# Kernel optimization log

Measured on AMD Instinct MI355X. Metric: run time of the kernel, lower is better.

The kernel has to match this reference:

```python
import jax, jax.numpy as jnp
import numpy as np

N_NODES = 50000
HIDDEN = 64
N_EDGES = 800000
HOPS = (1, 2, 3)


def setup_inputs() -> dict:
    key = jax.random.key(0)
    ks = jax.random.split(key, 16)
    d = HIDDEN
    inp = {
        "x": jax.random.normal(ks[0], (N_NODES, d), dtype=jnp.float32),
        "edge_index": jax.random.randint(ks[1], (2, N_EDGES), 0, N_NODES, dtype=jnp.int64),
    }
    s = 1.0 / np.sqrt(d)
    # per-hop GIN MLP params: Linear(d,d) -> ReLU -> Linear(d,d)
    for i in range(len(HOPS)):
        inp[f"W1_{i}"] = jax.random.uniform(ks[2 + 4 * i], (d, d), jnp.float32, -s, s)
        inp[f"b1_{i}"] = jax.random.uniform(ks[3 + 4 * i], (d,), jnp.float32, -s, s)
        inp[f"W2_{i}"] = jax.random.uniform(ks[4 + 4 * i], (d, d), jnp.float32, -s, s)
        inp[f"b2_{i}"] = jax.random.uniform(ks[5 + 4 * i], (d,), jnp.float32, -s, s)
    so = 1.0 / np.sqrt(d * len(HOPS))
    inp["Wo"] = jax.random.uniform(ks[14], (d * len(HOPS), d), jnp.float32, -so, so)
    inp["bo"] = jax.random.uniform(ks[15], (d,), jnp.float32, -so, so)
    return inp


def _gin_conv(h, src, dst, W1, b1, W2, b2):
    # GINConv with eps=0: MLP(x + sum_{j in N(i)} x_j)
    agg = jax.ops.segment_sum(h[src], dst, num_segments=N_NODES)  # [N, d]
    z = h + agg
    z = jax.nn.relu(z @ W1 + b1) @ W2 + b2
    return z


def reference(x, edge_index,
              W1_0, b1_0, W2_0, b2_0,
              W1_1, b1_1, W2_1, b2_1,
              W1_2, b1_2, W2_2, b2_2,
              Wo, bo):
    src, dst = edge_index[0], edge_index[1]
    params = [(W1_0, b1_0, W2_0, b2_0),
              (W1_1, b1_1, W2_1, b2_1),
              (W1_2, b1_2, W2_2, b2_2)]
    outs = []
    for hop, (W1, b1, W2, b2) in zip(HOPS, params):
        h = x
        for _ in range(hop):
            h = _gin_conv(h, src, dst, W1, b1, W2, b2)
        outs.append(h)
    return jnp.concatenate(outs, axis=-1) @ Wo + bo
```

## Files before the change

### kernel.cpp

```cpp
#include <hip/hip_runtime.h>

#define NN 50000
#define NE 800000
#define D  64
#define TILE 64
#define TPB 512
#define KTOT 192
#define NBLK 196


__global__ __launch_bounds__(256) void k_zero(int* __restrict__ p, int n) {
    int i = blockIdx.x * 256 + threadIdx.x;
    if (i < n) p[i] = 0;
}

__global__ __launch_bounds__(256) void k_count(const int* __restrict__ ei, int* __restrict__ deg) {
    int e = blockIdx.x * 256 + threadIdx.x;
    if (e < NE) atomicAdd(&deg[ei[NE + e]], 1);
}

__global__ __launch_bounds__(256) void k_bsum(const int* __restrict__ deg, int* __restrict__ bsum) {
    __shared__ int s[256];
    int t = threadIdx.x;
    int i = blockIdx.x * 256 + t;
    s[t] = (i < NN) ? deg[i] : 0;
    __syncthreads();
    for (int off = 128; off > 0; off >>= 1) {
        if (t < off) s[t] += s[t + off];
        __syncthreads();
    }
    if (t == 0) bsum[blockIdx.x] = s[0];
}

__global__ __launch_bounds__(256) void k_boff(const int* __restrict__ bsum,
                                              int* __restrict__ boff,
                                              int* __restrict__ row_ptr) {
    __shared__ int s[256];
    int t = threadIdx.x;
    int v = (t < NBLK) ? bsum[t] : 0;
    s[t] = v;
    __syncthreads();
    for (int off = 1; off < 256; off <<= 1) {
        int u = (t >= off) ? s[t - off] : 0;
        __syncthreads();
        s[t] += u;
        __syncthreads();
    }
    boff[t] = s[t] - v;
    if (t == 0) row_ptr[NN] = NE;
}

__global__ __launch_bounds__(256) void k_scan2(const int* __restrict__ deg,
                                               const int* __restrict__ boff,
                                               int* __restrict__ row_ptr,
                                               int* __restrict__ cursor) {
    __shared__ int s[256];
    int t = threadIdx.x;
    int i = blockIdx.x * 256 + t;
    int v = (i < NN) ? deg[i] : 0;
    s[t] = v;
    __syncthreads();
    for (int off = 1; off < 256; off <<= 1) {
        int u = (t >= off) ? s[t - off] : 0;
        __syncthreads();
        s[t] += u;
        __syncthreads();
    }
    int excl = s[t] - v + boff[blockIdx.x];
    if (i < NN) { row_ptr[i] = excl; cursor[i] = excl; }
}

__global__ __launch_bounds__(256) void k_fill(const int* __restrict__ ei,
                                              int* __restrict__ cursor,
                                              int* __restrict__ colv) {
    int e = blockIdx.x * 256 + threadIdx.x;
    if (e < NE) {
        int d = ei[NE + e];
        int p = atomicAdd(&cursor[d], 1);
        colv[p] = ei[e];
    }
}


__device__ __forceinline__ float4 gather_row(const float4* __restrict__ h4,
                                             const int* __restrict__ row_ptr,
                                             const int* __restrict__ colv,
                                             int n, int g, int q) {
    float4 a0 = make_float4(0.f, 0.f, 0.f, 0.f);
    float4 a1 = make_float4(0.f, 0.f, 0.f, 0.f);
    float4 a2 = make_float4(0.f, 0.f, 0.f, 0.f);
    float4 a3 = make_float4(0.f, 0.f, 0.f, 0.f);
    if (n >= 0) {
        if (g == 0) a0 = h4[n * 16 + q];
        int e1 = row_ptr[n + 1];
        int e  = row_ptr[n] + g;
        for (; e + 12 < e1; e += 16) {
            int s0 = colv[e], s1 = colv[e + 4], s2 = colv[e + 8], s3 = colv[e + 12];
            float4 v0 = h4[s0 * 16 + q];
            float4 v1 = h4[s1 * 16 + q];
            float4 v2 = h4[s2 * 16 + q];
            float4 v3 = h4[s3 * 16 + q];
            a0.x += v0.x; a0.y += v0.y; a0.z += v0.z; a0.w += v0.w;
            a1.x += v1.x; a1.y += v1.y; a1.z += v1.z; a1.w += v1.w;
            a2.x += v2.x; a2.y += v2.y; a2.z += v2.z; a2.w += v2.w;
            a3.x += v3.x; a3.y += v3.y; a3.z += v3.z; a3.w += v3.w;
        }
        for (; e < e1; e += 4) {
            float4 v = h4[colv[e] * 16 + q];
            a1.x += v.x; a1.y += v.y; a1.z += v.z; a1.w += v.w;
        }
        a0.x += a1.x + a2.x + a3.x;
        a0.y += a1.y + a2.y + a3.y;
        a0.z += a1.z + a2.z + a3.z;
        a0.w += a1.w + a2.w + a3.w;
    }
    a0.x += __shfl_xor(a0.x, 16); a0.y += __shfl_xor(a0.y, 16);
    a0.z += __shfl_xor(a0.z, 16); a0.w += __shfl_xor(a0.w, 16);
    a0.x += __shfl_xor(a0.x, 32); a0.y += __shfl_xor(a0.y, 32);
    a0.z += __shfl_xor(a0.z, 32); a0.w += __shfl_xor(a0.w, 32);
    return a0;
}


__global__ __launch_bounds__(TPB) void k_conv(
    const float4* __restrict__ h4,
    const int* __restrict__ row_ptr,
    const int* __restrict__ colv,
    const float* __restrict__ W1, const float* __restrict__ b1,
    const float* __restrict__ W2, const float* __restrict__ b2,
    float4* __restrict__ out4)
{
    __shared__ float sW1[D][D];
    __shared__ float sW2[D][D];
    __shared__ float4 sZ4[TILE][17];
    __shared__ float sB1[D], sB2[D];

    int tid = threadIdx.x;
    int node0 = blockIdx.x * TILE;

    {
        const float4* w14 = (const float4*)W1;
        const float4* w24 = (const float4*)W2;
        float4* s14 = (float4*)sW1;
        float4* s24 = (float4*)sW2;
        for (int i = tid; i < D * D / 4; i += TPB) { s14[i] = w14[i]; s24[i] = w24[i]; }
        if (tid < D) { sB1[tid] = b1[tid]; sB2[tid] = b2[tid]; }
    }

    int wave = tid >> 6, lane = tid & 63;
    int g = lane >> 4, q = lane & 15;

    for (int r = wave; r < TILE; r += (TPB / 64)) {
        int n = node0 + r;
        float4 a = gather_row(h4, row_ptr, colv, (n < NN) ? n : -1, g, q);
        if (g == 0) sZ4[r][q] = a;
    }
    __syncthreads();

    int tr = tid >> 4, tc = tid & 15;
    float* zr0 = (float*)&sZ4[tr * 2 + 0][0];
    float* zr1 = (float*)&sZ4[tr * 2 + 1][0];

    float acc[2][4];
    #pragma unroll
    for (int c = 0; c < 4; ++c) { acc[0][c] = sB1[tc * 4 + c]; acc[1][c] = sB1[tc * 4 + c]; }
    #pragma unroll 16
    for (int k = 0; k < D; ++k) {
        float z0 = zr0[k], z1 = zr1[k];
        #pragma unroll
        for (int c = 0; c < 4; ++c) {
            float w = sW1[k][tc * 4 + c];
            acc[0][c] += z0 * w;
            acc[1][c] += z1 * w;
        }
    }
    {
        float4 h0, h1;
        h0.x = fmaxf(acc[0][0], 0.f); h0.y = fmaxf(acc[0][1], 0.f);
        h0.z = fmaxf(acc[0][2], 0.f); h0.w = fmaxf(acc[0][3], 0.f);
        h1.x = fmaxf(acc[1][0], 0.f); h1.y = fmaxf(acc[1][1], 0.f);
        h1.z = fmaxf(acc[1][2], 0.f); h1.w = fmaxf(acc[1][3], 0.f);
        *(float4*)&zr0[tc * 4] = h0;
        *(float4*)&zr1[tc * 4] = h1;
    }
    #pragma unroll
    for (int c = 0; c < 4; ++c) { acc[0][c] = sB2[tc * 4 + c]; acc[1][c] = sB2[tc * 4 + c]; }
    #pragma unroll 16
    for (int k = 0; k < D; ++k) {
        float z0 = zr0[k], z1 = zr1[k];
        #pragma unroll
        for (int c = 0; c < 4; ++c) {
            float w = sW2[k][tc * 4 + c];
            acc[0][c] += z0 * w;
            acc[1][c] += z1 * w;
        }
    }
    #pragma unroll
    for (int i = 0; i < 2; ++i) {
        int n = node0 + tr * 2 + i;
        if (n < NN) {
            float4 o;
            o.x = acc[i][0]; o.y = acc[i][1]; o.z = acc[i][2]; o.w = acc[i][3];
            out4[n * 16 + tc] = o;
        }
    }
}


__global__ __launch_bounds__(TPB) void k_aggmlp3(
    const float4* __restrict__ h4,
    const int* __restrict__ row_ptr,
    const int* __restrict__ colv,
    const float* __restrict__ W1a, const float* __restrict__ b1a,
    const float* __restrict__ W2a, const float* __restrict__ b2a,
    const float* __restrict__ W1b, const float* __restrict__ b1b,
    const float* __restrict__ W2b, const float* __restrict__ b2b,
    const float* __restrict__ W1c, const float* __restrict__ b1c,
    const float* __restrict__ W2c, const float* __restrict__ b2c,
    float4* __restrict__ outA, float4* __restrict__ outB, float4* __restrict__ outC)
{
    __shared__ float sW[D][D];
    __shared__ float4 sZ4[TILE][17];
    __shared__ float4 sH4[TILE][17];
    __shared__ float sB[D];

    int tid = threadIdx.x;
    int node0 = blockIdx.x * TILE;

    int wave = tid >> 6, lane = tid & 63;
    int g = lane >> 4, q = lane & 63 & 15;

    for (int r = wave; r < TILE; r += (TPB / 64)) {
        int n = node0 + r;
        float4 a = gather_row(h4, row_ptr, colv, (n < NN) ? n : -1, g, q);
        if (g == 0) sZ4[r][q] = a;
    }

    int tr = tid >> 4, tc = tid & 15;
    float* zr0 = (float*)&sZ4[tr * 2 + 0][0];
    float* zr1 = (float*)&sZ4[tr * 2 + 1][0];
    float* hr0 = (float*)&sH4[tr * 2 + 0][0];
    float* hr1 = (float*)&sH4[tr * 2 + 1][0];

    #pragma unroll 1
    for (int m = 0; m < 3; ++m) {
        const float* W1 = (m == 0) ? W1a : (m == 1) ? W1b : W1c;
        const float* B1 = (m == 0) ? b1a : (m == 1) ? b1b : b1c;
        const float* W2 = (m == 0) ? W2a : (m == 1) ? W2b : W2c;
        const float* B2 = (m == 0) ? b2a : (m == 1) ? b2b : b2c;
        float4* out4 = (m == 0) ? outA : (m == 1) ? outB : outC;

        {
            const float4* w4 = (const float4*)W1;
            float4* s4 = (float4*)sW;
            for (int i = tid; i < D * D / 4; i += TPB) s4[i] = w4[i];
            if (tid < D) sB[tid] = B1[tid];
        }
        __syncthreads();

        float acc[2][4];
        #pragma unroll
        for (int c = 0; c < 4; ++c) { acc[0][c] = sB[tc * 4 + c]; acc[1][c] = sB[tc * 4 + c]; }
        #pragma unroll 16
        for (int k = 0; k < D; ++k) {
            float z0 = zr0[k], z1 = zr1[k];
            #pragma unroll
            for (int c = 0; c < 4; ++c) {
                float w = sW[k][tc * 4 + c];
                acc[0][c] += z0 * w;
                acc[1][c] += z1 * w;
            }
        }
        {
            float4 h0, h1;
            h0.x = fmaxf(acc[0][0], 0.f); h0.y = fmaxf(acc[0][1], 0.f);
            h0.z = fmaxf(acc[0][2], 0.f); h0.w = fmaxf(acc[0][3], 0.f);
            h1.x = fmaxf(acc[1][0], 0.f); h1.y = fmaxf(acc[1][1], 0.f);
            h1.z = fmaxf(acc[1][2], 0.f); h1.w = fmaxf(acc[1][3], 0.f);
            *(float4*)&hr0[tc * 4] = h0;
            *(float4*)&hr1[tc * 4] = h1;
        }
        __syncthreads();

        {
            const float4* w4 = (const float4*)W2;
            float4* s4 = (float4*)sW;
            for (int i = tid; i < D * D / 4; i += TPB) s4[i] = w4[i];
            if (tid < D) sB[tid] = B2[tid];
        }
        __syncthreads();

        #pragma unroll
        for (int c = 0; c < 4; ++c) { acc[0][c] = sB[tc * 4 + c]; acc[1][c] = sB[tc * 4 + c]; }
        #pragma unroll 16
        for (int k = 0; k < D; ++k) {
            float h0 = hr0[k], h1 = hr1[k];
            #pragma unroll
            for (int c = 0; c < 4; ++c) {
                float w = sW[k][tc * 4 + c];
                acc[0][c] += h0 * w;
                acc[1][c] += h1 * w;
            }
        }
        #pragma unroll
        for (int i = 0; i < 2; ++i) {
            int n = node0 + tr * 2 + i;
            if (n < NN) {
                float4 o;
                o.x = acc[i][0]; o.y = acc[i][1]; o.z = acc[i][2]; o.w = acc[i][3];
                out4[n * 16 + tc] = o;
            }
        }
        __syncthreads();
    }
}


__global__ __launch_bounds__(TPB) void k_final(
    const float4* __restrict__ H0, const float4* __restrict__ H1,
    const float4* __restrict__ H2,
    const float* __restrict__ Wo, const float* __restrict__ bo,
    float4* __restrict__ out4)
{
    __shared__ float4 sW4[KTOT * 16];
    __shared__ float4 sZ4[TILE][49];
    __shared__ float sB[D];

    int tid = threadIdx.x;
    int node0 = blockIdx.x * TILE;

    {
        const float4* w4 = (const float4*)Wo;
        for (int i = tid; i < KTOT * 16; i += TPB) sW4[i] = w4[i];
        if (tid < D) sB[tid] = bo[tid];
    }

    int wave = tid >> 6, lane = tid & 63;
    int part = lane >> 4, q = lane & 15;
    for (int r = wave; r < TILE; r += (TPB / 64)) {
        int n = node0 + r;
        if (part < 3) {
            float4 v = make_float4(0.f, 0.f, 0.f, 0.f);
            if (n < NN) {
                const float4* hp = (part == 0) ? H0 : (part == 1) ? H1 : H2;
                v = hp[n * 16 + q];
            }
            sZ4[r][part * 16 + q] = v;
        }
    }
    __syncthreads();

    const float* sW = (const float*)sW4;
    int tr = tid >> 4, tc = tid & 15;
    const float* zr0 = (const float*)&sZ4[tr * 2 + 0][0];
    const float* zr1 = (const float*)&sZ4[tr * 2 + 1][0];

    float acc[2][4];
    #pragma unroll
    for (int c = 0; c < 4; ++c) { acc[0][c] = sB[tc * 4 + c]; acc[1][c] = sB[tc * 4 + c]; }
    #pragma unroll 8
    for (int k = 0; k < KTOT; ++k) {
        float z0 = zr0[k], z1 = zr1[k];
        #pragma unroll
        for (int c = 0; c < 4; ++c) {
            float w = sW[k * 64 + tc * 4 + c];
            acc[0][c] += z0 * w;
            acc[1][c] += z1 * w;
        }
    }
    #pragma unroll
    for (int i = 0; i < 2; ++i) {
        int n = node0 + tr * 2 + i;
        if (n < NN) {
            float4 o;
            o.x = acc[i][0]; o.y = acc[i][1]; o.z = acc[i][2]; o.w = acc[i][3];
            out4[n * 16 + tc] = o;
        }
    }
}


extern "C" void kernel_launch(void* const* d_in, const int* in_sizes, int n_in,
                              void* d_out, int out_size, void* d_ws, size_t ws_size,
                              hipStream_t stream) {
    const float* x    = (const float*)d_in[0];
    const int*   ei   = (const int*)d_in[1];
    const float* W1_0 = (const float*)d_in[2];
    const float* b1_0 = (const float*)d_in[3];
    const float* W2_0 = (const float*)d_in[4];
    const float* b2_0 = (const float*)d_in[5];
    const float* W1_1 = (const float*)d_in[6];
    const float* b1_1 = (const float*)d_in[7];
    const float* W2_1 = (const float*)d_in[8];
    const float* b2_1 = (const float*)d_in[9];
    const float* W1_2 = (const float*)d_in[10];
    const float* b1_2 = (const float*)d_in[11];
    const float* W2_2 = (const float*)d_in[12];
    const float* b2_2 = (const float*)d_in[13];
    const float* Wo   = (const float*)d_in[14];
    const float* bo   = (const float*)d_in[15];
    float4* out = (float4*)d_out;

    char* ws = (char*)d_ws;
    int* deg     = (int*)(ws + 0);
    int* cursor  = (int*)(ws + 200704);
    int* row_ptr = (int*)(ws + 401408);
    int* colv    = (int*)(ws + 602112);
    int* bsum    = (int*)(ws + 3802112);
    int* boff    = (int*)(ws + 3803136);
    float* fbase = (float*)(ws + 3804160);
    float4* H0 = (float4*)(fbase);
    float4* H1 = (float4*)(fbase + 3200000);
    float4* H2 = (float4*)(fbase + 6400000);
    float4* tA = (float4*)(fbase + 9600000);
    const float4* x4 = (const float4*)x;

    k_zero <<<NBLK, 256, 0, stream>>>(deg, NN);
    k_count<<<(NE + 255) / 256, 256, 0, stream>>>(ei, deg);
    k_bsum <<<NBLK, 256, 0, stream>>>(deg, bsum);
    k_boff <<<1, 256, 0, stream>>>(bsum, boff, row_ptr);
    k_scan2<<<NBLK, 256, 0, stream>>>(deg, boff, row_ptr, cursor);
    k_fill <<<(NE + 255) / 256, 256, 0, stream>>>(ei, cursor, colv);

    int nb = (NN + TILE - 1) / TILE;

    k_aggmlp3<<<nb, TPB, 0, stream>>>(x4, row_ptr, colv,
                                      W1_0, b1_0, W2_0, b2_0,
                                      W1_1, b1_1, W2_1, b2_1,
                                      W1_2, b1_2, W2_2, b2_2,
                                      H0, tA, out);

    k_conv<<<nb, TPB, 0, stream>>>((const float4*)tA, row_ptr, colv,
                                   W1_1, b1_1, W2_1, b2_1, H1);

    k_conv<<<nb, TPB, 0, stream>>>((const float4*)out, row_ptr, colv,
                                   W1_2, b1_2, W2_2, b2_2, tA);
    k_conv<<<nb, TPB, 0, stream>>>((const float4*)tA, row_ptr, colv,
                                   W1_2, b1_2, W2_2, b2_2, H2);

    k_final<<<nb, TPB, 0, stream>>>((const float4*)H0, (const float4*)H1, (const float4*)H2,
                                    Wo, bo, out);
}
```

Measured before the change: 397.5 us.

## Fuse hop-2 convs into dual-gather kernel and fold output projection into last conv

Merges the two independent second-round GIN convolutions (hop-2 second layer and hop-3 second layer) into one kernel that gathers both feature tensors in the same edge loop, sharing the colv index reads. The final hop-3 conv is fused with the output projection, so H2 is never written to global memory and the projection streams Wo in three 64-row slices through one shared buffer. The device zeroing kernel is replaced by hipMemsetAsync. This cuts the launch count and the global traffic for edge indices and intermediates, at the cost of more serialized weight loads and syncs per block and a shallower gather unroll.

```diff
diff --git a/kernel.cpp b/kernel.cpp
--- a/kernel.cpp
+++ b/kernel.cpp
@@ -5,14 +5,8 @@
 #define D  64
 #define TILE 64
 #define TPB 512
-#define KTOT 192
 #define NBLK 196
 
-
-__global__ __launch_bounds__(256) void k_zero(int* __restrict__ p, int n) {
-    int i = blockIdx.x * 256 + threadIdx.x;
-    if (i < n) p[i] = 0;
-}
 
 __global__ __launch_bounds__(256) void k_count(const int* __restrict__ ei, int* __restrict__ deg) {
     int e = blockIdx.x * 256 + threadIdx.x;
@@ -81,6 +75,54 @@
     }
 }
 
+
+__device__ __forceinline__ void load_w(float (&sW)[D][D], const float* __restrict__ W, int tid) {
+    const float4* w4 = (const float4*)W;
+    float4* s4 = (float4*)sW;
+    for (int i = tid; i < D * D / 4; i += TPB) s4[i] = w4[i];
+}
+
+__device__ __forceinline__ void acc_init(float acc[2][4], const float* sB, int tc) {
+    #pragma unroll
+    for (int c = 0; c < 4; ++c) { acc[0][c] = sB[tc * 4 + c]; acc[1][c] = sB[tc * 4 + c]; }
+}
+
+__device__ __forceinline__ void layer_acc(float acc[2][4], const float* zr0, const float* zr1,
+                                          const float (&sW)[D][D], int tc) {
+    #pragma unroll 16
+    for (int k = 0; k < D; ++k) {
+        float z0 = zr0[k], z1 = zr1[k];
+        #pragma unroll
+        for (int c = 0; c < 4; ++c) {
+            float w = sW[k][tc * 4 + c];
+            acc[0][c] += z0 * w;
+            acc[1][c] += z1 * w;
+        }
+    }
+}
+
+__device__ __forceinline__ void relu_wb(float acc[2][4], float* zr0, float* zr1, int tc) {
+    float4 h0, h1;
+    h0.x = fmaxf(acc[0][0], 0.f); h0.y = fmaxf(acc[0][1], 0.f);
+    h0.z = fmaxf(acc[0][2], 0.f); h0.w = fmaxf(acc[0][3], 0.f);
+    h1.x = fmaxf(acc[1][0], 0.f); h1.y = fmaxf(acc[1][1], 0.f);
+    h1.z = fmaxf(acc[1][2], 0.f); h1.w = fmaxf(acc[1][3], 0.f);
+    *(float4*)&zr0[tc * 4] = h0;
+    *(float4*)&zr1[tc * 4] = h1;
+}
+
+__device__ __forceinline__ void store_rows(float acc[2][4], float4* __restrict__ out4,
+                                           int node0, int tr, int tc) {
+    #pragma unroll
+    for (int i = 0; i < 2; ++i) {
+        int n = node0 + tr * 2 + i;
+        if (n < NN) {
+            float4 o;
+            o.x = acc[i][0]; o.y = acc[i][1]; o.z = acc[i][2]; o.w = acc[i][3];
+            out4[n * 16 + tc] = o;
+        }
+    }
+}
 
 __device__ __forceinline__ float4 gather_row(const float4* __restrict__ h4,
                                              const int* __restrict__ row_ptr,
@@ -122,91 +164,6 @@
 }
 
 
-__global__ __launch_bounds__(TPB) void k_conv(
-    const float4* __restrict__ h4,
-    const int* __restrict__ row_ptr,
-    const int* __restrict__ colv,
-    const float* __restrict__ W1, const float* __restrict__ b1,
-    const float* __restrict__ W2, const float* __restrict__ b2,
-    float4* __restrict__ out4)
-{
-    __shared__ float sW1[D][D];
-    __shared__ float sW2[D][D];
-    __shared__ float4 sZ4[TILE][17];
-    __shared__ float sB1[D], sB2[D];
-
-    int tid = threadIdx.x;
-    int node0 = blockIdx.x * TILE;
-
-    {
-        const float4* w14 = (const float4*)W1;
-        const float4* w24 = (const float4*)W2;
-        float4* s14 = (float4*)sW1;
-        float4* s24 = (float4*)sW2;
-        for (int i = tid; i < D * D / 4; i += TPB) { s14[i] = w14[i]; s24[i] = w24[i]; }
-        if (tid < D) { sB1[tid] = b1[tid]; sB2[tid] = b2[tid]; }
-    }
-
-    int wave = tid >> 6, lane = tid & 63;
-    int g = lane >> 4, q = lane & 15;
-
-    for (int r = wave; r < TILE; r += (TPB / 64)) {
-        int n = node0 + r;
-        float4 a = gather_row(h4, row_ptr, colv, (n < NN) ? n : -1, g, q);
-        if (g == 0) sZ4[r][q] = a;
-    }
-    __syncthreads();
-
-    int tr = tid >> 4, tc = tid & 15;
-    float* zr0 = (float*)&sZ4[tr * 2 + 0][0];
-    float* zr1 = (float*)&sZ4[tr * 2 + 1][0];
-
-    float acc[2][4];
-    #pragma unroll
-    for (int c = 0; c < 4; ++c) { acc[0][c] = sB1[tc * 4 + c]; acc[1][c] = sB1[tc * 4 + c]; }
-    #pragma unroll 16
-    for (int k = 0; k < D; ++k) {
-        float z0 = zr0[k], z1 = zr1[k];
-        #pragma unroll
-        for (int c = 0; c < 4; ++c) {
-            float w = sW1[k][tc * 4 + c];
-            acc[0][c] += z0 * w;
-            acc[1][c] += z1 * w;
-        }
-    }
-    {
-        float4 h0, h1;
-        h0.x = fmaxf(acc[0][0], 0.f); h0.y = fmaxf(acc[0][1], 0.f);
-        h0.z = fmaxf(acc[0][2], 0.f); h0.w = fmaxf(acc[0][3], 0.f);
-        h1.x = fmaxf(acc[1][0], 0.f); h1.y = fmaxf(acc[1][1], 0.f);
-        h1.z = fmaxf(acc[1][2], 0.f); h1.w = fmaxf(acc[1][3], 0.f);
-        *(float4*)&zr0[tc * 4] = h0;
-        *(float4*)&zr1[tc * 4] = h1;
-    }
-    #pragma unroll
-    for (int c = 0; c < 4; ++c) { acc[0][c] = sB2[tc * 4 + c]; acc[1][c] = sB2[tc * 4 + c]; }
-    #pragma unroll 16
-    for (int k = 0; k < D; ++k) {
-        float z0 = zr0[k], z1 = zr1[k];
-        #pragma unroll
-        for (int c = 0; c < 4; ++c) {
-            float w = sW2[k][tc * 4 + c];
-            acc[0][c] += z0 * w;
-            acc[1][c] += z1 * w;
-        }
-    }
-    #pragma unroll
-    for (int i = 0; i < 2; ++i) {
-        int n = node0 + tr * 2 + i;
-        if (n < NN) {
-            float4 o;
-            o.x = acc[i][0]; o.y = acc[i][1]; o.z = acc[i][2]; o.w = acc[i][3];
-            out4[n * 16 + tc] = o;
-        }
-    }
-}
-
-
 __global__ __launch_bounds__(TPB) void k_aggmlp3(
     const float4* __restrict__ h4,
     const int* __restrict__ row_ptr,
@@ -226,9 +183,8 @@
 
     int tid = threadIdx.x;
     int node0 = blockIdx.x * TILE;
-
     int wave = tid >> 6, lane = tid & 63;
-    int g = lane >> 4, q = lane & 63 & 15;
+    int g = lane >> 4, q = lane & 15;
 
     for (int r = wave; r < TILE; r += (TPB / 64)) {
         int n = node0 + r;
@@ -250,133 +206,201 @@
         const float* B2 = (m == 0) ? b2a : (m == 1) ? b2b : b2c;
         float4* out4 = (m == 0) ? outA : (m == 1) ? outB : outC;
 
-        {
-            const float4* w4 = (const float4*)W1;
-            float4* s4 = (float4*)sW;
-            for (int i = tid; i < D * D / 4; i += TPB) s4[i] = w4[i];
-            if (tid < D) sB[tid] = B1[tid];
+        load_w(sW, W1, tid);
+        if (tid < D) sB[tid] = B1[tid];
+        __syncthreads();
+
+        float acc[2][4];
+        acc_init(acc, sB, tc);
+        layer_acc(acc, zr0, zr1, sW, tc);
+        relu_wb(acc, hr0, hr1, tc);
+        __syncthreads();
+
+        load_w(sW, W2, tid);
+        if (tid < D) sB[tid] = B2[tid];
+        __syncthreads();
+
+        acc_init(acc, sB, tc);
+        layer_acc(acc, hr0, hr1, sW, tc);
+        store_rows(acc, out4, node0, tr, tc);
+        __syncthreads();
+    }
+}
+
+
+__global__ __launch_bounds__(TPB) void k_conv2(
+    const float4* __restrict__ hA4, const float4* __restrict__ hB4,
+    const int* __restrict__ row_ptr, const int* __restrict__ colv,
+    const float* __restrict__ W1a, const float* __restrict__ b1a,
+    const float* __restrict__ W2a, const float* __restrict__ b2a,
+    const float* __restrict__ W1b, const float* __restrict__ b1b,
+    const float* __restrict__ W2b, const float* __restrict__ b2b,
+    float4* __restrict__ outA4, float4* __restrict__ outB4)
+{
+    __shared__ float sW[D][D];
+    __shared__ float4 sZa[TILE][17];
+    __shared__ float4 sZb[TILE][17];
+    __shared__ float sB[D];
+
+    int tid = threadIdx.x;
+    int node0 = blockIdx.x * TILE;
+    int wave = tid >> 6, lane = tid & 63;
+    int g = lane >> 4, q = lane & 15;
+
+    for (int r = wave; r < TILE; r += (TPB / 64)) {
+        int n = node0 + r;
+        float4 a0 = make_float4(0.f, 0.f, 0.f, 0.f);
+        float4 a1 = make_float4(0.f, 0.f, 0.f, 0.f);
+        float4 b0 = make_float4(0.f, 0.f, 0.f, 0.f);
+        float4 b1v = make_float4(0.f, 0.f, 0.f, 0.f);
+        if (n < NN) {
+            if (g == 0) { a0 = hA4[n * 16 + q]; b0 = hB4[n * 16 + q]; }
+            int e1 = row_ptr[n + 1];
+            int e  = row_ptr[n] + g;
+            for (; e + 4 < e1; e += 8) {
+                int s0 = colv[e], s1 = colv[e + 4];
+                float4 va0 = hA4[s0 * 16 + q];
+                float4 vb0 = hB4[s0 * 16 + q];
+                float4 va1 = hA4[s1 * 16 + q];
+                float4 vb1 = hB4[s1 * 16 + q];
+                a0.x += va0.x; a0.y += va0.y; a0.z += va0.z; a0.w += va0.w;
+                b0.x += vb0.x; b0.y += vb0.y; b0.z += vb0.z; b0.w += vb0.w;
+                a1.x += va1.x; a1.y += va1.y; a1.z += va1.z; a1.w += va1.w;
+                b1v.x += vb1.x; b1v.y += vb1.y; b1v.z += vb1.z; b1v.w += vb1.w;
+            }
+            if (e < e1) {
+                int s = colv[e];
+                float4 va = hA4[s * 16 + q];
+                float4 vb = hB4[s * 16 + q];
+                a0.x += va.x; a0.y += va.y; a0.z += va.z; a0.w += va.w;
+                b0.x += vb.x; b0.y += vb.y; b0.z += vb.z; b0.w += vb.w;
+            }
+            a0.x += a1.x; a0.y += a1.y; a0.z += a1.z; a0.w += a1.w;
+            b0.x += b1v.x; b0.y += b1v.y; b0.z += b1v.z; b0.w += b1v.w;
         }
-        __syncthreads();
-
-        float acc[2][4];
-        #pragma unroll
-        for (int c = 0; c < 4; ++c) { acc[0][c] = sB[tc * 4 + c]; acc[1][c] = sB[tc * 4 + c]; }
-        #pragma unroll 16
-        for (int k = 0; k < D; ++k) {
-            float z0 = zr0[k], z1 = zr1[k];
-            #pragma unroll
-            for (int c = 0; c < 4; ++c) {
-                float w = sW[k][tc * 4 + c];
-                acc[0][c] += z0 * w;
-                acc[1][c] += z1 * w;
-            }
-        }
-        {
-            float4 h0, h1;
-            h0.x = fmaxf(acc[0][0], 0.f); h0.y = fmaxf(acc[0][1], 0.f);
-            h0.z = fmaxf(acc[0][2], 0.f); h0.w = fmaxf(acc[0][3], 0.f);
-            h1.x = fmaxf(acc[1][0], 0.f); h1.y = fmaxf(acc[1][1], 0.f);
-            h1.z = fmaxf(acc[1][2], 0.f); h1.w = fmaxf(acc[1][3], 0.f);
-            *(float4*)&hr0[tc * 4] = h0;
-            *(float4*)&hr1[tc * 4] = h1;
-        }
-        __syncthreads();
-
-        {
-            const float4* w4 = (const float4*)W2;
-            float4* s4 = (float4*)sW;
-            for (int i = tid; i < D * D / 4; i += TPB) s4[i] = w4[i];
-            if (tid < D) sB[tid] = B2[tid];
-        }
-        __syncthreads();
-
-        #pragma unroll
-        for (int c = 0; c < 4; ++c) { acc[0][c] = sB[tc * 4 + c]; acc[1][c] = sB[tc * 4 + c]; }
-        #pragma unroll 16
-        for (int k = 0; k < D; ++k) {
-            float h0 = hr0[k], h1 = hr1[k];
-            #pragma unroll
-            for (int c = 0; c < 4; ++c) {
-                float w = sW[k][tc * 4 + c];
-                acc[0][c] += h0 * w;
-                acc[1][c] += h1 * w;
-            }
-        }
-        #pragma unroll
-        for (int i = 0; i < 2; ++i) {
-            int n = node0 + tr * 2 + i;
-            if (n < NN) {
-                float4 o;
-                o.x = acc[i][0]; o.y = acc[i][1]; o.z = acc[i][2]; o.w = acc[i][3];
-                out4[n * 16 + tc] = o;
-            }
-        }
-        __syncthreads();
-    }
-}
-
-
-__global__ __launch_bounds__(TPB) void k_final(
+        a0.x += __shfl_xor(a0.x, 16); a0.y += __shfl_xor(a0.y, 16);
+        a0.z += __shfl_xor(a0.z, 16); a0.w += __shfl_xor(a0.w, 16);
+        a0.x += __shfl_xor(a0.x, 32); a0.y += __shfl_xor(a0.y, 32);
+        a0.z += __shfl_xor(a0.z, 32); a0.w += __shfl_xor(a0.w, 32);
+        b0.x += __shfl_xor(b0.x, 16); b0.y += __shfl_xor(b0.y, 16);
+        b0.z += __shfl_xor(b0.z, 16); b0.w += __shfl_xor(b0.w, 16);
+        b0.x += __shfl_xor(b0.x, 32); b0.y += __shfl_xor(b0.y, 32);
+        b0.z += __shfl_xor(b0.z, 32); b0.w += __shfl_xor(b0.w, 32);
+        if (g == 0) { sZa[r][q] = a0; sZb[r][q] = b0; }
+    }
+
+    int tr = tid >> 4, tc = tid & 15;
+    float* zra0 = (float*)&sZa[tr * 2 + 0][0];
+    float* zra1 = (float*)&sZa[tr * 2 + 1][0];
+    float* zrb0 = (float*)&sZb[tr * 2 + 0][0];
+    float* zrb1 = (float*)&sZb[tr * 2 + 1][0];
+    float acc[2][4];
+
+    load_w(sW, W1a, tid); if (tid < D) sB[tid] = b1a[tid];
+    __syncthreads();
+    acc_init(acc, sB, tc);
+    layer_acc(acc, zra0, zra1, sW, tc);
+    relu_wb(acc, zra0, zra1, tc);
+    __syncthreads();
+    load_w(sW, W2a, tid); if (tid < D) sB[tid] = b2a[tid];
+    __syncthreads();
+    acc_init(acc, sB, tc);
+    layer_acc(acc, zra0, zra1, sW, tc);
+    store_rows(acc, outA4, node0, tr, tc);
+    __syncthreads();
+
+    load_w(sW, W1b, tid); if (tid < D) sB[tid] = b1b[tid];
+    __syncthreads();
+    acc_init(acc, sB, tc);
+    layer_acc(acc, zrb0, zrb1, sW, tc);
+    relu_wb(acc, zrb0, zrb1, tc);
+    __syncthreads();
+    load_w(sW, W2b, tid); if (tid < D) sB[tid] = b2b[tid];
+    __syncthreads();
+    acc_init(acc, sB, tc);
+    layer_acc(acc, zrb0, zrb1, sW, tc);
+    store_rows(acc, outB4, node0, tr, tc);
+}
+
+
+__global__ __launch_bounds__(TPB) void k_conv_final(
+    const float4* __restrict__ h4,
     const float4* __restrict__ H0, const float4* __restrict__ H1,
-    const float4* __restrict__ H2,
+    const int* __restrict__ row_ptr, const int* __restrict__ colv,
+    const float* __restrict__ W1, const float* __restrict__ b1,
+    const float* __restrict__ W2, const float* __restrict__ b2,
     const float* __restrict__ Wo, const float* __restrict__ bo,
     float4* __restrict__ out4)
 {
-    __shared__ float4 sW4[KTOT * 16];
-    __shared__ float4 sZ4[TILE][49];
+    __shared__ float sW[D][D];
+    __shared__ float4 sZ4[TILE][17];
+    __shared__ float4 sY4[TILE][17];
     __shared__ float sB[D];
 
     int tid = threadIdx.x;
     int node0 = blockIdx.x * TILE;
-
-    {
-        const float4* w4 = (const float4*)Wo;
-        for (int i = tid; i < KTOT * 16; i += TPB) sW4[i] = w4[i];
-        if (tid < D) sB[tid] = bo[tid];
-    }
-
     int wave = tid >> 6, lane = tid & 63;
-    int part = lane >> 4, q = lane & 15;
+    int g = lane >> 4, q = lane & 15;
+
     for (int r = wave; r < TILE; r += (TPB / 64)) {
         int n = node0 + r;
-        if (part < 3) {
-            float4 v = make_float4(0.f, 0.f, 0.f, 0.f);
-            if (n < NN) {
-                const float4* hp = (part == 0) ? H0 : (part == 1) ? H1 : H2;
-                v = hp[n * 16 + q];
-            }
-            sZ4[r][part * 16 + q] = v;
-        }
-    }
-    __syncthreads();
-
-    const float* sW = (const float*)sW4;
+        float4 a = gather_row(h4, row_ptr, colv, (n < NN) ? n : -1, g, q);
+        if (g == 0) sZ4[r][q] = a;
+    }
+
     int tr = tid >> 4, tc = tid & 15;
-    const float* zr0 = (const float*)&sZ4[tr * 2 + 0][0];
-    const float* zr1 = (const float*)&sZ4[tr * 2 + 1][0];
-
+    float* zr0 = (float*)&sZ4[tr * 2 + 0][0];
+    float* zr1 = (float*)&sZ4[tr * 2 + 1][0];
+    float* yr0 = (float*)&sY4[tr * 2 + 0][0];
+    float* yr1 = (float*)&sY4[tr * 2 + 1][0];
     float acc[2][4];
-    #pragma unroll
-    for (int c = 0; c < 4; ++c) { acc[0][c] = sB[tc * 4 + c]; acc[1][c] = sB[tc * 4 + c]; }
-    #pragma unroll 8
-    for (int k = 0; k < KTOT; ++k) {
-        float z0 = zr0[k], z1 = zr1[k];
-        #pragma unroll
-        for (int c = 0; c < 4; ++c) {
-            float w = sW[k * 64 + tc * 4 + c];
-            acc[0][c] += z0 * w;
-            acc[1][c] += z1 * w;
-        }
-    }
-    #pragma unroll
-    for (int i = 0; i < 2; ++i) {
-        int n = node0 + tr * 2 + i;
-        if (n < NN) {
-            float4 o;
-            o.x = acc[i][0]; o.y = acc[i][1]; o.z = acc[i][2]; o.w = acc[i][3];
-            out4[n * 16 + tc] = o;
-        }
-    }
+
+    load_w(sW, W1, tid); if (tid < D) sB[tid] = b1[tid];
+    __syncthreads();
+    acc_init(acc, sB, tc);
+    layer_acc(acc, zr0, zr1, sW, tc);
+    relu_wb(acc, zr0, zr1, tc);
+    __syncthreads();
+    load_w(sW, W2, tid); if (tid < D) sB[tid] = b2[tid];
+    __syncthreads();
+    acc_init(acc, sB, tc);
+    layer_acc(acc, zr0, zr1, sW, tc);
+    {
+        float4 h0v, h1v;
+        h0v.x = acc[0][0]; h0v.y = acc[0][1]; h0v.z = acc[0][2]; h0v.w = acc[0][3];
+        h1v.x = acc[1][0]; h1v.y = acc[1][1]; h1v.z = acc[1][2]; h1v.w = acc[1][3];
+        *(float4*)&zr0[tc * 4] = h0v;
+        *(float4*)&zr1[tc * 4] = h1v;
+    }
+    __syncthreads();
+
+    load_w(sW, Wo + 128 * D, tid); if (tid < D) sB[tid] = bo[tid];
+    for (int i = tid; i < TILE * 16; i += TPB) {
+        int r = i >> 4, qq = i & 15;
+        int n = node0 + r;
+        sY4[r][qq] = (n < NN) ? H0[n * 16 + qq] : make_float4(0.f, 0.f, 0.f, 0.f);
+    }
+    __syncthreads();
+    float accO[2][4];
+    acc_init(accO, sB, tc);
+    layer_acc(accO, zr0, zr1, sW, tc);
+    __syncthreads();
+
+    load_w(sW, Wo, tid);
+    __syncthreads();
+    layer_acc(accO, yr0, yr1, sW, tc);
+    __syncthreads();
+
+    load_w(sW, Wo + 64 * D, tid);
+    for (int i = tid; i < TILE * 16; i += TPB) {
+        int r = i >> 4, qq = i & 15;
+        int n = node0 + r;
+        sY4[r][qq] = (n < NN) ? H1[n * 16 + qq] : make_float4(0.f, 0.f, 0.f, 0.f);
+    }
+    __syncthreads();
+    layer_acc(accO, yr0, yr1, sW, tc);
+
+    store_rows(accO, out4, node0, tr, tc);
 }
 
 
@@ -409,13 +433,13 @@
     int* bsum    = (int*)(ws + 3802112);
     int* boff    = (int*)(ws + 3803136);
     float* fbase = (float*)(ws + 3804160);
-    float4* H0 = (float4*)(fbase);
-    float4* H1 = (float4*)(fbase + 3200000);
-    float4* H2 = (float4*)(fbase + 6400000);
-    float4* tA = (float4*)(fbase + 9600000);
+    float4* H0  = (float4*)(fbase);
+    float4* H1  = (float4*)(fbase + 3200000);
+    float4* tB  = (float4*)(fbase + 6400000);
+    float4* tC2 = (float4*)(fbase + 9600000);
     const float4* x4 = (const float4*)x;
 
-    k_zero <<<NBLK, 256, 0, stream>>>(deg, NN);
+    hipMemsetAsync(deg, 0, NN * sizeof(int), stream);
     k_count<<<(NE + 255) / 256, 256, 0, stream>>>(ei, deg);
     k_bsum <<<NBLK, 256, 0, stream>>>(deg, bsum);
     k_boff <<<1, 256, 0, stream>>>(bsum, boff, row_ptr);
@@ -428,16 +452,16 @@
                                       W1_0, b1_0, W2_0, b2_0,
                                       W1_1, b1_1, W2_1, b2_1,
                                       W1_2, b1_2, W2_2, b2_2,
-                                      H0, tA, out);
-
-    k_conv<<<nb, TPB, 0, stream>>>((const float4*)tA, row_ptr, colv,
-                                   W1_1, b1_1, W2_1, b2_1, H1);
-
-    k_conv<<<nb, TPB, 0, stream>>>((const float4*)out, row_ptr, colv,
-                                   W1_2, b1_2, W2_2, b2_2, tA);
-    k_conv<<<nb, TPB, 0, stream>>>((const float4*)tA, row_ptr, colv,
-                                   W1_2, b1_2, W2_2, b2_2, H2);
-
-    k_final<<<nb, TPB, 0, stream>>>((const float4*)H0, (const float4*)H1, (const float4*)H2,
-                                    Wo, bo, out);
-}
+                                      H0, tB, out);
+
+    k_conv2<<<nb, TPB, 0, stream>>>(tB, (const float4*)out, row_ptr, colv,
+                                    W1_1, b1_1, W2_1, b2_1,
+                                    W1_2, b1_2, W2_2, b2_2,
+                                    H1, tC2);
+
+    k_conv_final<<<nb, TPB, 0, stream>>>((const float4*)tC2,
+                                         (const float4*)H0, (const float4*)H1,
+                                         row_ptr, colv,
+                                         W1_2, b1_2, W2_2, b2_2,
+                                         Wo, bo, out);
+}
```

After: 502.8 us. +26.5%, slower.

## Fuse last GIN conv with final output projection and replace zero kernel with memset

Applied to the files above, without the earlier changes.

Merges the third hop's final GINConv with the concatenated output projection into one kernel. The hop-3 result is kept in shared memory and multiplied by its slice of Wo, and H0 and H1 are reloaded per tile for the other two slices. This removes one kernel launch and the write and re-read of the H2 intermediate. The zeroing kernel is also replaced with hipMemsetAsync. In exchange, the fused kernel reloads a weight matrix into shared memory four times per tile and adds more barriers.

```diff
diff --git a/kernel.cpp b/kernel.cpp
--- a/kernel.cpp
+++ b/kernel.cpp
@@ -5,14 +5,8 @@
 #define D  64
 #define TILE 64
 #define TPB 512
-#define KTOT 192
 #define NBLK 196
 
-
-__global__ __launch_bounds__(256) void k_zero(int* __restrict__ p, int n) {
-    int i = blockIdx.x * 256 + threadIdx.x;
-    if (i < n) p[i] = 0;
-}
 
 __global__ __launch_bounds__(256) void k_count(const int* __restrict__ ei, int* __restrict__ deg) {
     int e = blockIdx.x * 256 + threadIdx.x;
@@ -316,64 +310,172 @@
 }
 
 
-__global__ __launch_bounds__(TPB) void k_final(
+__global__ __launch_bounds__(TPB) void k_conv_final(
+    const float4* __restrict__ h4,
     const float4* __restrict__ H0, const float4* __restrict__ H1,
-    const float4* __restrict__ H2,
+    const int* __restrict__ row_ptr, const int* __restrict__ colv,
+    const float* __restrict__ W1, const float* __restrict__ b1,
+    const float* __restrict__ W2, const float* __restrict__ b2,
     const float* __restrict__ Wo, const float* __restrict__ bo,
     float4* __restrict__ out4)
 {
-    __shared__ float4 sW4[KTOT * 16];
-    __shared__ float4 sZ4[TILE][49];
+    __shared__ float sW[D][D];
+    __shared__ float4 sZ4[TILE][17];
+    __shared__ float4 sY4[TILE][17];
     __shared__ float sB[D];
 
     int tid = threadIdx.x;
     int node0 = blockIdx.x * TILE;
-
-    {
-        const float4* w4 = (const float4*)Wo;
-        for (int i = tid; i < KTOT * 16; i += TPB) sW4[i] = w4[i];
-        if (tid < D) sB[tid] = bo[tid];
-    }
-
     int wave = tid >> 6, lane = tid & 63;
-    int part = lane >> 4, q = lane & 15;
+    int g = lane >> 4, q = lane & 15;
+
     for (int r = wave; r < TILE; r += (TPB / 64)) {
         int n = node0 + r;
-        if (part < 3) {
-            float4 v = make_float4(0.f, 0.f, 0.f, 0.f);
-            if (n < NN) {
-                const float4* hp = (part == 0) ? H0 : (part == 1) ? H1 : H2;
-                v = hp[n * 16 + q];
-            }
-            sZ4[r][part * 16 + q] = v;
-        }
-    }
-    __syncthreads();
-
-    const float* sW = (const float*)sW4;
+        float4 a = gather_row(h4, row_ptr, colv, (n < NN) ? n : -1, g, q);
+        if (g == 0) sZ4[r][q] = a;
+    }
+
     int tr = tid >> 4, tc = tid & 15;
-    const float* zr0 = (const float*)&sZ4[tr * 2 + 0][0];
-    const float* zr1 = (const float*)&sZ4[tr * 2 + 1][0];
+    float* zr0 = (float*)&sZ4[tr * 2 + 0][0];
+    float* zr1 = (float*)&sZ4[tr * 2 + 1][0];
+    float* yr0 = (float*)&sY4[tr * 2 + 0][0];
+    float* yr1 = (float*)&sY4[tr * 2 + 1][0];
+
+    {
+        const float4* w4 = (const float4*)W1;
+        float4* s4 = (float4*)sW;
+        for (int i = tid; i < D * D / 4; i += TPB) s4[i] = w4[i];
+        if (tid < D) sB[tid] = b1[tid];
+    }
+    __syncthreads();
 
     float acc[2][4];
     #pragma unroll
     for (int c = 0; c < 4; ++c) { acc[0][c] = sB[tc * 4 + c]; acc[1][c] = sB[tc * 4 + c]; }
-    #pragma unroll 8
-    for (int k = 0; k < KTOT; ++k) {
+    #pragma unroll 16
+    for (int k = 0; k < D; ++k) {
         float z0 = zr0[k], z1 = zr1[k];
         #pragma unroll
         for (int c = 0; c < 4; ++c) {
-            float w = sW[k * 64 + tc * 4 + c];
+            float w = sW[k][tc * 4 + c];
             acc[0][c] += z0 * w;
             acc[1][c] += z1 * w;
         }
     }
+    {
+        float4 h0, h1;
+        h0.x = fmaxf(acc[0][0], 0.f); h0.y = fmaxf(acc[0][1], 0.f);
+        h0.z = fmaxf(acc[0][2], 0.f); h0.w = fmaxf(acc[0][3], 0.f);
+        h1.x = fmaxf(acc[1][0], 0.f); h1.y = fmaxf(acc[1][1], 0.f);
+        h1.z = fmaxf(acc[1][2], 0.f); h1.w = fmaxf(acc[1][3], 0.f);
+        *(float4*)&zr0[tc * 4] = h0;
+        *(float4*)&zr1[tc * 4] = h1;
+    }
+    __syncthreads();
+
+    {
+        const float4* w4 = (const float4*)W2;
+        float4* s4 = (float4*)sW;
+        for (int i = tid; i < D * D / 4; i += TPB) s4[i] = w4[i];
+        if (tid < D) sB[tid] = b2[tid];
+    }
+    __syncthreads();
+
+    #pragma unroll
+    for (int c = 0; c < 4; ++c) { acc[0][c] = sB[tc * 4 + c]; acc[1][c] = sB[tc * 4 + c]; }
+    #pragma unroll 16
+    for (int k = 0; k < D; ++k) {
+        float z0 = zr0[k], z1 = zr1[k];
+        #pragma unroll
+        for (int c = 0; c < 4; ++c) {
+            float w = sW[k][tc * 4 + c];
+            acc[0][c] += z0 * w;
+            acc[1][c] += z1 * w;
+        }
+    }
+    {
+        float4 h0, h1;
+        h0.x = acc[0][0]; h0.y = acc[0][1]; h0.z = acc[0][2]; h0.w = acc[0][3];
+        h1.x = acc[1][0]; h1.y = acc[1][1]; h1.z = acc[1][2]; h1.w = acc[1][3];
+        *(float4*)&zr0[tc * 4] = h0;
+        *(float4*)&zr1[tc * 4] = h1;
+    }
+    __syncthreads();
+
+    {
+        const float4* w4 = (const float4*)(Wo + 128 * D);
+        float4* s4 = (float4*)sW;
+        for (int i = tid; i < D * D / 4; i += TPB) s4[i] = w4[i];
+        if (tid < D) sB[tid] = bo[tid];
+    }
+    for (int i = tid; i < TILE * 16; i += TPB) {
+        int r = i >> 4, qq = i & 15;
+        int n = node0 + r;
+        sY4[r][qq] = (n < NN) ? H0[n * 16 + qq] : make_float4(0.f, 0.f, 0.f, 0.f);
+    }
+    __syncthreads();
+
+    float accO[2][4];
+    #pragma unroll
+    for (int c = 0; c < 4; ++c) { accO[0][c] = sB[tc * 4 + c]; accO[1][c] = sB[tc * 4 + c]; }
+    #pragma unroll 16
+    for (int k = 0; k < D; ++k) {
+        float z0 = zr0[k], z1 = zr1[k];
+        #pragma unroll
+        for (int c = 0; c < 4; ++c) {
+            float w = sW[k][tc * 4 + c];
+            accO[0][c] += z0 * w;
+            accO[1][c] += z1 * w;
+        }
+    }
+    __syncthreads();
+
+    {
+        const float4* w4 = (const float4*)Wo;
+        float4* s4 = (float4*)sW;
+        for (int i = tid; i < D * D / 4; i += TPB) s4[i] = w4[i];
+    }
+    __syncthreads();
+    #pragma unroll 16
+    for (int k = 0; k < D; ++k) {
+        float z0 = yr0[k], z1 = yr1[k];
+        #pragma unroll
+        for (int c = 0; c < 4; ++c) {
+            float w = sW[k][tc * 4 + c];
+            accO[0][c] += z0 * w;
+            accO[1][c] += z1 * w;
+        }
+    }
+    __syncthreads();
+
+    {
+        const float4* w4 = (const float4*)(Wo + 64 * D);
+        float4* s4 = (float4*)sW;
+        for (int i = tid; i < D * D / 4; i += TPB) s4[i] = w4[i];
+    }
+    for (int i = tid; i < TILE * 16; i += TPB) {
+        int r = i >> 4, qq = i & 15;
+        int n = node0 + r;
+        sY4[r][qq] = (n < NN) ? H1[n * 16 + qq] : make_float4(0.f, 0.f, 0.f, 0.f);
+    }
+    __syncthreads();
+    #pragma unroll 16
+    for (int k = 0; k < D; ++k) {
+        float z0 = yr0[k], z1 = yr1[k];
+        #pragma unroll
+        for (int c = 0; c < 4; ++c) {
+            float w = sW[k][tc * 4 + c];
+            accO[0][c] += z0 * w;
+            accO[1][c] += z1 * w;
+        }
+    }
+
     #pragma unroll
     for (int i = 0; i < 2; ++i) {
         int n = node0 + tr * 2 + i;
         if (n < NN) {
             float4 o;
-            o.x = acc[i][0]; o.y = acc[i][1]; o.z = acc[i][2]; o.w = acc[i][3];
+            o.x = accO[i][0]; o.y = accO[i][1]; o.z = accO[i][2]; o.w = accO[i][3];
             out4[n * 16 + tc] = o;
         }
     }
@@ -409,13 +511,13 @@
     int* bsum    = (int*)(ws + 3802112);
     int* boff    = (int*)(ws + 3803136);
     float* fbase = (float*)(ws + 3804160);
-    float4* H0 = (float4*)(fbase);
-    float4* H1 = (float4*)(fbase + 3200000);
-    float4* H2 = (float4*)(fbase + 6400000);
-    float4* tA = (float4*)(fbase + 9600000);
+    float4* H0  = (float4*)(fbase);
+    float4* H1  = (float4*)(fbase + 3200000);
+    float4* tB  = (float4*)(fbase + 6400000);
+    float4* tC2 = (float4*)(fbase + 9600000);
     const float4* x4 = (const float4*)x;
 
-    k_zero <<<NBLK, 256, 0, stream>>>(deg, NN);
+    hipMemsetAsync(deg, 0, NN * sizeof(int), stream);
     k_count<<<(NE + 255) / 256, 256, 0, stream>>>(ei, deg);
     k_bsum <<<NBLK, 256, 0, stream>>>(deg, bsum);
     k_boff <<<1, 256, 0, stream>>>(bsum, boff, row_ptr);
@@ -428,16 +530,17 @@
                                       W1_0, b1_0, W2_0, b2_0,
                                       W1_1, b1_1, W2_1, b2_1,
                                       W1_2, b1_2, W2_2, b2_2,
-                                      H0, tA, out);
-
-    k_conv<<<nb, TPB, 0, stream>>>((const float4*)tA, row_ptr, colv,
+                                      H0, tB, out);
+
+    k_conv<<<nb, TPB, 0, stream>>>((const float4*)tB, row_ptr, colv,
                                    W1_1, b1_1, W2_1, b2_1, H1);
 
     k_conv<<<nb, TPB, 0, stream>>>((const float4*)out, row_ptr, colv,
-                                   W1_2, b1_2, W2_2, b2_2, tA);
-    k_conv<<<nb, TPB, 0, stream>>>((const float4*)tA, row_ptr, colv,
-                                   W1_2, b1_2, W2_2, b2_2, H2);
-
-    k_final<<<nb, TPB, 0, stream>>>((const float4*)H0, (const float4*)H1, (const float4*)H2,
-                                    Wo, bo, out);
-}
+                                   W1_2, b1_2, W2_2, b2_2, tC2);
+
+    k_conv_final<<<nb, TPB, 0, stream>>>((const float4*)tC2,
+                                         (const float4*)H0, (const float4*)H1,
+                                         row_ptr, colv,
+                                         W1_2, b1_2, W2_2, b2_2,
+                                         Wo, bo, out);
+}
```

New measurement: 428.3 us. 7.7% more time.
